# Performance work log

Measured on AMD Instinct MI355X. Metric: run time of the kernel, lower is better.

Reference implementation:

```python
import jax, jax.numpy as jnp
import numpy as np

B = 32768   # batch
D = 64      # latent_dimension_half
H = 256     # inner_dimension
T = D * (D + 1) // 2  # 2080 triangular outputs


def setup_inputs() -> dict:
    key = jax.random.key(0)
    ks = jax.random.split(key, 7)
    s = 0.05
    return {
        "x": jax.random.normal(ks[0], (B, D), dtype=jnp.float32),
        "W1": jax.random.normal(ks[1], (D, H), dtype=jnp.float32) * s,
        "b1": jax.random.normal(ks[2], (H,), dtype=jnp.float32) * s,
        "W2": jax.random.normal(ks[3], (H, H), dtype=jnp.float32) * s,
        "b2": jax.random.normal(ks[4], (H,), dtype=jnp.float32) * s,
        "W3": jax.random.normal(ks[5], (H, T), dtype=jnp.float32) * s,
        "b3": jax.random.normal(ks[6], (T,), dtype=jnp.float32) * s,
    }


def reference(x, W1, b1, W2, b2, W3, b3):
    d = x.shape[-1]  # latent_dimension_half
    h = jnp.tanh(x @ W1 + b1)
    h = jnp.tanh(h @ W2 + b2)
    t = jnp.tanh(h @ W3 + b3)  # [B, d*(d+1)/2]
    # scatter: first d entries -> diagonal (diagflat), rest -> strict upper
    # triangle in row-major order (matches torch boolean-mask assignment)
    di = np.arange(d)
    iu, ju = np.triu_indices(d, k=1)
    rows = np.concatenate([di, iu])
    cols = np.concatenate([di, ju])
    u = jnp.zeros((x.shape[0], d, d), dtype=t.dtype).at[:, rows, cols].set(t)
    # y[b] = u[b].T @ u[b]
    return jnp.einsum('bki,bkj->bij', u, u)
```

## Files before the change

kernel.cpp:

```cpp
#include <hip/hip_runtime.h>


typedef __bf16 bf16_t;
typedef bf16_t bf16x8 __attribute__((ext_vector_type(8)));
typedef float  f32x4  __attribute__((ext_vector_type(4)));

#define MFMA16(a, b, c) __builtin_amdgcn_mfma_f32_16x16x32_bf16((a), (b), (c), 0, 0, 0)

constexpr int SLOT  = 4608;
constexpr int ARENA = 73728;
constexpr int H2OFF = 147456;

__device__ __forceinline__ float fast_tanh(float x) {
  float cx = fminf(fmaxf(x, -30.0f), 30.0f);
  float t  = __expf(2.0f * cx);
  return (t - 1.0f) * __builtin_amdgcn_rcpf(t + 1.0f);
}

__device__ __forceinline__ bf16x8 zsel(bf16x8 f, bool keep) {
  union { bf16x8 v; unsigned int u[4]; } x;
  x.v = f;
  unsigned m = keep ? 0xFFFFFFFFu : 0u;
#pragma unroll
  for (int p = 0; p < 4; ++p) x.u[p] &= m;
  return x.v;
}

__device__ __forceinline__ void decode_p(int p, int& j, int& k) {
  int cc = p >> 3, e = p & 7;
  int b = 0;
  while (b < 7 && cc >= 4 * (b + 1) * (b + 2)) ++b;
  int rl  = b + 1;
  int rem = cc - 4 * b * (b + 1);
  j = 8 * b + rem / rl;
  k = (rem % rl) * 8 + e;
}

__global__ void prep_kernel(const float* __restrict__ W1, const float* __restrict__ W2,
                            const float* __restrict__ W3, const float* __restrict__ b3,
                            char* __restrict__ wsb) {
  int tid = blockIdx.x * 512 + threadIdx.x;
  bf16_t* ws = (bf16_t*)wsb;
  if (tid < 16384) {
    int n = tid >> 6, k = tid & 63;
    ws[tid] = (bf16_t)W1[k * 256 + n];
  } else if (tid < 81920) {
    int m = tid - 16384;
    int n = m >> 8, k = m & 255;
    ws[tid] = (bf16_t)W2[k * 256 + n];
  } else if (tid < 671744) {
    int m = tid - 81920;
    int t  = m >> 12;
    int r  = m & 4095;
    int kk = r >> 9;
    int g  = (r >> 7) & 3;
    int c  = (r >> 3) & 15;
    int e  = r & 7;
    int p  = t * 16 + c;
    int k  = kk * 32 + g * 8 + e;
    int j, kd;
    decode_p(p, j, kd);
    float v = 0.f;
    if (kd <= j) {
      int n_ref = (kd == j) ? j : (64 + kd * 63 - (kd * (kd - 1)) / 2 + j - kd - 1);
      v = W3[k * 2080 + n_ref];
    }
    ws[tid] = (bf16_t)v;
  } else if (tid < 674048) {
    int p = tid - 671744;
    int j, kd;
    decode_p(p, j, kd);
    float v = 0.f;
    if (kd <= j) {
      int n_ref = (kd == j) ? j : (64 + kd * 63 - (kd * (kd - 1)) / 2 + j - kd - 1);
      v = b3[n_ref];
    }
    ((float*)(wsb + 1343488))[p] = v;
  }
}

__device__ __forceinline__ void gram_store(char* slot, int sw, float* yb,
                                           int g, int c, int lane) {
  bf16x8 f0, f1, f2, f3, f2b, f3b;
#pragma unroll
  for (int ti = 0; ti < 4; ++ti) {
    int j = ti * 16 + c;
    int Q = j >> 3, s = j & 7;
    int ro = 16 * (4 * Q * (Q + 1) + s * (Q + 1));
    bf16x8 fa = *(const bf16x8*)(slot + ((ro + g * 16) ^ sw));
    if (ti == 0) f0 = zsel(fa, g * 8 <= j);
    if (ti == 1) f1 = zsel(fa, g * 8 <= j);
    if (ti == 2) f2 = fa;
    if (ti == 3) f3 = fa;
    if (ti >= 2) {
      bf16x8 fb = *(const bf16x8*)(slot + ((ro + 64 + g * 16) ^ sw));
      fb = zsel(fb, 32 + g * 8 <= j);
      if (ti == 2) f2b = fb;
      else         f3b = fb;
    }
  }

  bf16x8 fA[4] = {f0, f1, f2, f3};
  f32x4 acc[4][4];
#pragma unroll
  for (int ti = 0; ti < 4; ++ti)
#pragma unroll
    for (int tj = 0; tj < 4; ++tj) {
      f32x4 z = {0.f, 0.f, 0.f, 0.f};
      acc[ti][tj] = MFMA16(fA[ti], fA[tj], z);
    }
  acc[2][2] = MFMA16(f2b, f2b, acc[2][2]);
  acc[2][3] = MFMA16(f2b, f3b, acc[2][3]);
  acc[3][2] = MFMA16(f3b, f2b, acc[3][2]);
  acc[3][3] = MFMA16(f3b, f3b, acc[3][3]);

#pragma unroll
  for (int ti = 0; ti < 4; ++ti) {
#pragma unroll
    for (int tj = 0; tj < 4; ++tj)
#pragma unroll
      for (int r = 0; r < 4; ++r)
        *(float*)(slot + (g * 4 + r) * 256 + (tj * 16 + c) * 4) = acc[ti][tj][r];
#pragma unroll
    for (int ii = 0; ii < 4; ++ii) {
      f32x4 v = *(const f32x4*)(slot + ii * 1024 + lane * 16);
      __builtin_nontemporal_store(v, (f32x4*)(yb + ti * 1024 + ii * 256 + lane * 4));
    }
  }
}

__global__ void __launch_bounds__(768, 3)
hm_kernel(const float* __restrict__ x, const float* __restrict__ b1,
          const float* __restrict__ b2, const char* __restrict__ wsb,
          float* __restrict__ out) {
  extern __shared__ char smem[];
  const int tid  = threadIdx.x;
  const int w    = tid >> 6;
  const int lane = tid & 63;
  const int g    = lane >> 4;
  const int c    = lane & 15;
  const int blk  = blockIdx.x;

  const bf16_t* W1t = (const bf16_t*)wsb;
  const bf16_t* W2t = W1t + 16384;
  const bf16_t* W3q = W1t + 81920;
  const float*  b3p = (const float*)(wsb + 1343488);
  char* h2s = smem + H2OFF;

  float bias1[2] = {0.f, 0.f}, bias2[2] = {0.f, 0.f};
  if (w < 8) {
#pragma unroll
    for (int ni = 0; ni < 2; ++ni) {
      int n = (w * 2 + ni) * 16 + c;
      bias1[ni] = b1[n];
      bias2[ni] = b2[n];
    }
  }

#pragma unroll 1
  for (int r = 0; r < 8; ++r) {
    char* cur = smem + (r & 1) * ARENA;
    char* prv = smem + ((r & 1) ^ 1) * ARENA;
    char* xs  = cur;
    char* h1s = cur + 4096;

    if (tid < 256) {
      f32x4 v = *(const f32x4*)(x + ((size_t)blk * 128 + r * 16) * 64 + tid * 4);
      int row = tid >> 4, col = (tid & 15) * 4;
      union { bf16_t b[4]; unsigned long long u; } pk;
      pk.b[0] = (bf16_t)v[0]; pk.b[1] = (bf16_t)v[1];
      pk.b[2] = (bf16_t)v[2]; pk.b[3] = (bf16_t)v[3];
      *(unsigned long long*)(xs + ((row * 128 + col * 2) ^ ((row & 7) << 4))) = pk.u;
    }
    __syncthreads();

    if (w < 8) {
      bf16x8 a0 = *(const bf16x8*)(xs + ((c * 128 + g * 16) ^ ((c & 7) << 4)));
      bf16x8 a1 = *(const bf16x8*)(xs + ((c * 128 + 64 + g * 16) ^ ((c & 7) << 4)));
#pragma unroll
      for (int ni = 0; ni < 2; ++ni) {
        int n = (w * 2 + ni) * 16 + c;
        bf16x8 bw0 = *(const bf16x8*)(W1t + n * 64 + g * 8);
        bf16x8 bw1 = *(const bf16x8*)(W1t + n * 64 + 32 + g * 8);
        f32x4 acc = {0.f, 0.f, 0.f, 0.f};
        acc = MFMA16(a0, bw0, acc);
        acc = MFMA16(a1, bw1, acc);
#pragma unroll
        for (int rr = 0; rr < 4; ++rr) {
          int row = g * 4 + rr;
          float v = fast_tanh(acc[rr] + bias1[ni]);
          *(bf16_t*)(h1s + ((row * 512 + n * 2) ^ ((row & 7) << 4))) = (bf16_t)v;
        }
      }
    }
    __syncthreads();

    if (w < 8) {
#pragma unroll
      for (int ni = 0; ni < 2; ++ni) {
        int n = (w * 2 + ni) * 16 + c;
        f32x4 acc0 = {0.f, 0.f, 0.f, 0.f}, acc1 = {0.f, 0.f, 0.f, 0.f};
#pragma unroll
        for (int kk = 0; kk < 8; kk += 2) {
          bf16x8 a0 = *(const bf16x8*)(h1s + ((c * 512 + kk * 64 + g * 16) ^ ((c & 7) << 4)));
          bf16x8 a1 = *(const bf16x8*)(h1s + ((c * 512 + (kk + 1) * 64 + g * 16) ^ ((c & 7) << 4)));
          bf16x8 bw0 = *(const bf16x8*)(W2t + n * 256 + kk * 32 + g * 8);
          bf16x8 bw1 = *(const bf16x8*)(W2t + n * 256 + (kk + 1) * 32 + g * 8);
          acc0 = MFMA16(a0, bw0, acc0);
          acc1 = MFMA16(a1, bw1, acc1);
        }
        f32x4 acc = acc0 + acc1;
#pragma unroll
        for (int rr = 0; rr < 4; ++rr) {
          int row = g * 4 + rr;
          float v = fast_tanh(acc[rr] + bias2[ni]);
          *(bf16_t*)(h2s + ((row * 512 + n * 2) ^ ((row & 7) << 4))) = (bf16_t)v;
        }
      }
    }
    __syncthreads();

    if (w < 8) {
      bf16x8 a0 = *(const bf16x8*)(h2s + ((c * 512 + 0 * 64 + g * 16) ^ ((c & 7) << 4)));
      bf16x8 a1 = *(const bf16x8*)(h2s + ((c * 512 + 1 * 64 + g * 16) ^ ((c & 7) << 4)));
      bf16x8 a2 = *(const bf16x8*)(h2s + ((c * 512 + 2 * 64 + g * 16) ^ ((c & 7) << 4)));
      bf16x8 a3 = *(const bf16x8*)(h2s + ((c * 512 + 3 * 64 + g * 16) ^ ((c & 7) << 4)));
      bf16x8 a4 = *(const bf16x8*)(h2s + ((c * 512 + 4 * 64 + g * 16) ^ ((c & 7) << 4)));
      bf16x8 a5 = *(const bf16x8*)(h2s + ((c * 512 + 5 * 64 + g * 16) ^ ((c & 7) << 4)));
      bf16x8 a6 = *(const bf16x8*)(h2s + ((c * 512 + 6 * 64 + g * 16) ^ ((c & 7) << 4)));
      bf16x8 a7 = *(const bf16x8*)(h2s + ((c * 512 + 7 * 64 + g * 16) ^ ((c & 7) << 4)));

      char* tw = cur + (g * 4) * SLOT;
      const int swz = (g & 7) << 4;

      bf16x8 A0, A1, A2, A3, A4, A5, A6, A7; float Ab;
      bf16x8 B0, B1, B2, B3, B4, B5, B6, B7; float Bb;

#define ISSUE_T(S, TI)                                                              \
  do {                                                                              \
    int t_ = w + (TI) * 8;                                                          \
    const bf16_t* np_ = W3q + t_ * 4096 + lane * 8;                                 \
    asm volatile("global_load_dwordx4 %0, %1, off" : "=v"(S##0) : "v"(np_));            \
    asm volatile("global_load_dwordx4 %0, %1, off" : "=v"(S##1) : "v"(np_ + 512));      \
    asm volatile("global_load_dwordx4 %0, %1, off" : "=v"(S##2) : "v"(np_ + 1024));     \
    asm volatile("global_load_dwordx4 %0, %1, off" : "=v"(S##3) : "v"(np_ + 1536));     \
    asm volatile("global_load_dwordx4 %0, %1, off" : "=v"(S##4) : "v"(np_ + 2048));     \
    asm volatile("global_load_dwordx4 %0, %1, off" : "=v"(S##5) : "v"(np_ + 2560));     \
    asm volatile("global_load_dwordx4 %0, %1, off" : "=v"(S##6) : "v"(np_ + 3072));     \
    asm volatile("global_load_dwordx4 %0, %1, off" : "=v"(S##7) : "v"(np_ + 3584));     \
    asm volatile("global_load_dword %0, %1, off"   : "=v"(S##b) : "v"(b3p + t_ * 16 + c)); \
  } while (0)

#define WAIT_N(N)                                          \
  do {                                                     \
    asm volatile("s_waitcnt vmcnt(" #N ")" ::: "memory");  \
    __builtin_amdgcn_sched_barrier(0);                     \
  } while (0)

#define COMP_T(S, TI)                                                    \
  do {                                                                   \
    f32x4 acc0 = {S##b, S##b, S##b, S##b};                               \
    f32x4 acc1 = {0.f, 0.f, 0.f, 0.f};                                   \
    acc0 = MFMA16(a0, S##0, acc0); acc1 = MFMA16(a1, S##1, acc1);        \
    acc0 = MFMA16(a2, S##2, acc0); acc1 = MFMA16(a3, S##3, acc1);        \
    acc0 = MFMA16(a4, S##4, acc0); acc1 = MFMA16(a5, S##5, acc1);        \
    acc0 = MFMA16(a6, S##6, acc0); acc1 = MFMA16(a7, S##7, acc1);        \
    f32x4 accs = acc0 + acc1;                                            \
    int p_ = (w + (TI) * 8) * 16 + c;                                    \
    _Pragma("unroll")                                                    \
    for (int r_ = 0; r_ < 4; ++r_) {                                     \
      float v_ = fast_tanh(accs[r_]);                                    \
      *(bf16_t*)(tw + r_ * SLOT + ((p_ * 2) ^ swz)) = (bf16_t)v_;        \
    }                                                                    \
  } while (0)

      ISSUE_T(A, 0);
#pragma unroll 1
      for (int pr = 0; pr < 8; ++pr) {
        ISSUE_T(B, 2 * pr + 1);
        WAIT_N(9);
        COMP_T(A, 2 * pr);
        ISSUE_T(A, 2 * pr + 2);
        WAIT_N(9);
        COMP_T(B, 2 * pr + 1);
      }
      ISSUE_T(B, 17);
      WAIT_N(9);
      COMP_T(A, 16);
      WAIT_N(0);
      COMP_T(B, 17);

#undef ISSUE_T
#undef WAIT_N
#undef COMP_T
    } else if (r > 0) {
      int ww = w - 8;
#pragma unroll 1
      for (int bi = 0; bi < 4; ++bi) {
        int m = ww * 4 + bi;
        gram_store(prv + m * SLOT, ((m >> 2) & 7) << 4,
                   out + ((size_t)blk * 128 + (r - 1) * 16 + m) * 4096,
                   g, c, lane);
      }
    }
    __syncthreads();
  }

  if (w < 8) {
#pragma unroll
    for (int bi = 0; bi < 2; ++bi) {
      int m = w * 2 + bi;
      gram_store(smem + ARENA + m * SLOT, ((m >> 2) & 7) << 4,
                 out + ((size_t)blk * 128 + 7 * 16 + m) * 4096,
                 g, c, lane);
    }
  }
}

extern "C" void kernel_launch(void* const* d_in, const int* in_sizes, int n_in,
                              void* d_out, int out_size, void* d_ws, size_t ws_size,
                              hipStream_t stream) {
  (void)in_sizes; (void)n_in; (void)out_size; (void)ws_size;
  const float* x  = (const float*)d_in[0];
  const float* W1 = (const float*)d_in[1];
  const float* b1 = (const float*)d_in[2];
  const float* W2 = (const float*)d_in[3];
  const float* b2 = (const float*)d_in[4];
  const float* W3 = (const float*)d_in[5];
  const float* b3 = (const float*)d_in[6];
  char* wsb = (char*)d_ws;
  float* out = (float*)d_out;

  prep_kernel<<<1317, 512, 0, stream>>>(W1, W2, W3, b3, wsb);

  hipFuncSetAttribute((const void*)hm_kernel,
                      hipFuncAttributeMaxDynamicSharedMemorySize, 155648);
  hm_kernel<<<256, 768, 155648, stream>>>(x, b1, b2, wsb, out);
}
```

Measured before the change: 207.3 us.

## Replace block-wide barriers with LDS counter flags between producer and consumer warps

Swaps the per-stage __syncthreads between MLP warps and gram-store warps for named LDS counters: the 8 compute warps sync among themselves with atomic arrive/spin-wait, and the 4 store warps wait on per-round ready flags and signal buffer release. This lets the MLP pipeline run ahead into the next round while the store warps drain the previous arena, removing lockstep stalls. It also moves the final-round store onto the store warps. The risks are spin-wait overhead (s_sleep polling), LDS atomic traffic, and subtle memory-ordering hazards if the waitcnt/fence placement is insufficient.

```diff
diff --git a/kernel.cpp b/kernel.cpp
--- a/kernel.cpp
+++ b/kernel.cpp
@@ -10,6 +10,7 @@
 constexpr int SLOT  = 4608;
 constexpr int ARENA = 73728;
 constexpr int H2OFF = 147456;
+constexpr int CTRL  = 155648;
 
 __device__ __forceinline__ float fast_tanh(float x) {
   float cx = fminf(fmaxf(x, -30.0f), 30.0f);
@@ -34,6 +35,16 @@
   int rem = cc - 4 * b * (b + 1);
   j = 8 * b + rem / rl;
   k = (rem % rl) * 8 + e;
+}
+
+__device__ __forceinline__ void lds_arrive(unsigned* p, int lane) {
+  asm volatile("s_waitcnt lgkmcnt(0)" ::: "memory");
+  if (lane == 0) atomicAdd(p, 1u);
+}
+__device__ __forceinline__ void lds_wait(volatile unsigned* p, unsigned tgt) {
+  while (*p < tgt) __builtin_amdgcn_s_sleep(2);
+  asm volatile("" ::: "memory");
+  __builtin_amdgcn_sched_barrier(0);
 }
 
 __global__ void prep_kernel(const float* __restrict__ W1, const float* __restrict__ W2,
@@ -146,56 +157,59 @@
   const bf16_t* W3q = W1t + 81920;
   const float*  b3p = (const float*)(wsb + 1343488);
   char* h2s = smem + H2OFF;
-
-  float bias1[2] = {0.f, 0.f}, bias2[2] = {0.f, 0.f};
+  unsigned* ctrl = (unsigned*)(smem + CTRL);
+
+  if (tid < 40) ctrl[tid] = 0;
+  __syncthreads();
+
   if (w < 8) {
+    float bias1[2], bias2[2];
 #pragma unroll
     for (int ni = 0; ni < 2; ++ni) {
       int n = (w * 2 + ni) * 16 + c;
       bias1[ni] = b1[n];
       bias2[ni] = b2[n];
     }
-  }
 
 #pragma unroll 1
-  for (int r = 0; r < 8; ++r) {
-    char* cur = smem + (r & 1) * ARENA;
-    char* prv = smem + ((r & 1) ^ 1) * ARENA;
-    char* xs  = cur;
-    char* h1s = cur + 4096;
-
-    if (tid < 256) {
-      f32x4 v = *(const f32x4*)(x + ((size_t)blk * 128 + r * 16) * 64 + tid * 4);
-      int row = tid >> 4, col = (tid & 15) * 4;
-      union { bf16_t b[4]; unsigned long long u; } pk;
-      pk.b[0] = (bf16_t)v[0]; pk.b[1] = (bf16_t)v[1];
-      pk.b[2] = (bf16_t)v[2]; pk.b[3] = (bf16_t)v[3];
-      *(unsigned long long*)(xs + ((row * 128 + col * 2) ^ ((row & 7) << 4))) = pk.u;
-    }
-    __syncthreads();
-
-    if (w < 8) {
-      bf16x8 a0 = *(const bf16x8*)(xs + ((c * 128 + g * 16) ^ ((c & 7) << 4)));
-      bf16x8 a1 = *(const bf16x8*)(xs + ((c * 128 + 64 + g * 16) ^ ((c & 7) << 4)));
-#pragma unroll
-      for (int ni = 0; ni < 2; ++ni) {
-        int n = (w * 2 + ni) * 16 + c;
-        bf16x8 bw0 = *(const bf16x8*)(W1t + n * 64 + g * 8);
-        bf16x8 bw1 = *(const bf16x8*)(W1t + n * 64 + 32 + g * 8);
-        f32x4 acc = {0.f, 0.f, 0.f, 0.f};
-        acc = MFMA16(a0, bw0, acc);
-        acc = MFMA16(a1, bw1, acc);
-#pragma unroll
-        for (int rr = 0; rr < 4; ++rr) {
-          int row = g * 4 + rr;
-          float v = fast_tanh(acc[rr] + bias1[ni]);
-          *(bf16_t*)(h1s + ((row * 512 + n * 2) ^ ((row & 7) << 4))) = (bf16_t)v;
+    for (int r = 0; r < 8; ++r) {
+      char* cur = smem + (r & 1) * ARENA;
+      char* xs  = cur;
+      char* h1s = cur + 4096;
+
+      if (r >= 2) lds_wait(&ctrl[32 + (r - 2)], 4);
+
+      if (tid < 256) {
+        f32x4 v = *(const f32x4*)(x + ((size_t)blk * 128 + r * 16) * 64 + tid * 4);
+        int row = tid >> 4, col = (tid & 15) * 4;
+        union { bf16_t b[4]; unsigned long long u; } pk;
+        pk.b[0] = (bf16_t)v[0]; pk.b[1] = (bf16_t)v[1];
+        pk.b[2] = (bf16_t)v[2]; pk.b[3] = (bf16_t)v[3];
+        *(unsigned long long*)(xs + ((row * 128 + col * 2) ^ ((row & 7) << 4))) = pk.u;
+      }
+      lds_arrive(&ctrl[r * 3 + 0], lane); lds_wait(&ctrl[r * 3 + 0], 8);
+
+      {
+        bf16x8 a0 = *(const bf16x8*)(xs + ((c * 128 + g * 16) ^ ((c & 7) << 4)));
+        bf16x8 a1 = *(const bf16x8*)(xs + ((c * 128 + 64 + g * 16) ^ ((c & 7) << 4)));
+#pragma unroll
+        for (int ni = 0; ni < 2; ++ni) {
+          int n = (w * 2 + ni) * 16 + c;
+          bf16x8 bw0 = *(const bf16x8*)(W1t + n * 64 + g * 8);
+          bf16x8 bw1 = *(const bf16x8*)(W1t + n * 64 + 32 + g * 8);
+          f32x4 acc = {0.f, 0.f, 0.f, 0.f};
+          acc = MFMA16(a0, bw0, acc);
+          acc = MFMA16(a1, bw1, acc);
+#pragma unroll
+          for (int rr = 0; rr < 4; ++rr) {
+            int row = g * 4 + rr;
+            float v = fast_tanh(acc[rr] + bias1[ni]);
+            *(bf16_t*)(h1s + ((row * 512 + n * 2) ^ ((row & 7) << 4))) = (bf16_t)v;
+          }
         }
       }
-    }
-    __syncthreads();
-
-    if (w < 8) {
+      lds_arrive(&ctrl[r * 3 + 1], lane); lds_wait(&ctrl[r * 3 + 1], 8);
+
 #pragma unroll
       for (int ni = 0; ni < 2; ++ni) {
         int n = (w * 2 + ni) * 16 + c;
@@ -217,24 +231,23 @@
           *(bf16_t*)(h2s + ((row * 512 + n * 2) ^ ((row & 7) << 4))) = (bf16_t)v;
         }
       }
-    }
-    __syncthreads();
-
-    if (w < 8) {
-      bf16x8 a0 = *(const bf16x8*)(h2s + ((c * 512 + 0 * 64 + g * 16) ^ ((c & 7) << 4)));
-      bf16x8 a1 = *(const bf16x8*)(h2s + ((c * 512 + 1 * 64 + g * 16) ^ ((c & 7) << 4)));
-      bf16x8 a2 = *(const bf16x8*)(h2s + ((c * 512 + 2 * 64 + g * 16) ^ ((c & 7) << 4)));
-      bf16x8 a3 = *(const bf16x8*)(h2s + ((c * 512 + 3 * 64 + g * 16) ^ ((c & 7) << 4)));
-      bf16x8 a4 = *(const bf16x8*)(h2s + ((c * 512 + 4 * 64 + g * 16) ^ ((c & 7) << 4)));
-      bf16x8 a5 = *(const bf16x8*)(h2s + ((c * 512 + 5 * 64 + g * 16) ^ ((c & 7) << 4)));
-      bf16x8 a6 = *(const bf16x8*)(h2s + ((c * 512 + 6 * 64 + g * 16) ^ ((c & 7) << 4)));
-      bf16x8 a7 = *(const bf16x8*)(h2s + ((c * 512 + 7 * 64 + g * 16) ^ ((c & 7) << 4)));
-
-      char* tw = cur + (g * 4) * SLOT;
-      const int swz = (g & 7) << 4;
-
-      bf16x8 A0, A1, A2, A3, A4, A5, A6, A7; float Ab;
-      bf16x8 B0, B1, B2, B3, B4, B5, B6, B7; float Bb;
+      lds_arrive(&ctrl[r * 3 + 2], lane); lds_wait(&ctrl[r * 3 + 2], 8);
+
+      {
+        bf16x8 a0 = *(const bf16x8*)(h2s + ((c * 512 + 0 * 64 + g * 16) ^ ((c & 7) << 4)));
+        bf16x8 a1 = *(const bf16x8*)(h2s + ((c * 512 + 1 * 64 + g * 16) ^ ((c & 7) << 4)));
+        bf16x8 a2 = *(const bf16x8*)(h2s + ((c * 512 + 2 * 64 + g * 16) ^ ((c & 7) << 4)));
+        bf16x8 a3 = *(const bf16x8*)(h2s + ((c * 512 + 3 * 64 + g * 16) ^ ((c & 7) << 4)));
+        bf16x8 a4 = *(const bf16x8*)(h2s + ((c * 512 + 4 * 64 + g * 16) ^ ((c & 7) << 4)));
+        bf16x8 a5 = *(const bf16x8*)(h2s + ((c * 512 + 5 * 64 + g * 16) ^ ((c & 7) << 4)));
+        bf16x8 a6 = *(const bf16x8*)(h2s + ((c * 512 + 6 * 64 + g * 16) ^ ((c & 7) << 4)));
+        bf16x8 a7 = *(const bf16x8*)(h2s + ((c * 512 + 7 * 64 + g * 16) ^ ((c & 7) << 4)));
+
+        char* tw = cur + (g * 4) * SLOT;
+        const int swz = (g & 7) << 4;
+
+        bf16x8 A0, A1, A2, A3, A4, A5, A6, A7; float Ab;
+        bf16x8 B0, B1, B2, B3, B4, B5, B6, B7; float Bb;
 
 #define ISSUE_T(S, TI)                                                              \
   do {                                                                              \
@@ -274,45 +287,42 @@
     }                                                                    \
   } while (0)
 
-      ISSUE_T(A, 0);
+        ISSUE_T(A, 0);
 #pragma unroll 1
-      for (int pr = 0; pr < 8; ++pr) {
-        ISSUE_T(B, 2 * pr + 1);
+        for (int pr = 0; pr < 8; ++pr) {
+          ISSUE_T(B, 2 * pr + 1);
+          WAIT_N(9);
+          COMP_T(A, 2 * pr);
+          ISSUE_T(A, 2 * pr + 2);
+          WAIT_N(9);
+          COMP_T(B, 2 * pr + 1);
+        }
+        ISSUE_T(B, 17);
         WAIT_N(9);
-        COMP_T(A, 2 * pr);
-        ISSUE_T(A, 2 * pr + 2);
-        WAIT_N(9);
-        COMP_T(B, 2 * pr + 1);
-      }
-      ISSUE_T(B, 17);
-      WAIT_N(9);
-      COMP_T(A, 16);
-      WAIT_N(0);
-      COMP_T(B, 17);
+        COMP_T(A, 16);
+        WAIT_N(0);
+        COMP_T(B, 17);
 
 #undef ISSUE_T
 #undef WAIT_N
 #undef COMP_T
-    } else if (r > 0) {
-      int ww = w - 8;
+      }
+      lds_arrive(&ctrl[24 + r], lane);
+    }
+  } else {
+    int ww = w - 8;
+#pragma unroll 1
+    for (int r = 0; r < 8; ++r) {
+      lds_wait(&ctrl[24 + r], 8);
+      char* arena = smem + (r & 1) * ARENA;
 #pragma unroll 1
       for (int bi = 0; bi < 4; ++bi) {
         int m = ww * 4 + bi;
-        gram_store(prv + m * SLOT, ((m >> 2) & 7) << 4,
-                   out + ((size_t)blk * 128 + (r - 1) * 16 + m) * 4096,
+        gram_store(arena + m * SLOT, ((m >> 2) & 7) << 4,
+                   out + ((size_t)blk * 128 + r * 16 + m) * 4096,
                    g, c, lane);
       }
-    }
-    __syncthreads();
-  }
-
-  if (w < 8) {
-#pragma unroll
-    for (int bi = 0; bi < 2; ++bi) {
-      int m = w * 2 + bi;
-      gram_store(smem + ARENA + m * SLOT, ((m >> 2) & 7) << 4,
-                 out + ((size_t)blk * 128 + 7 * 16 + m) * 4096,
-                 g, c, lane);
+      lds_arrive(&ctrl[32 + r], lane);
     }
   }
 }
@@ -334,6 +344,6 @@
   prep_kernel<<<1317, 512, 0, stream>>>(W1, W2, W3, b3, wsb);
 
   hipFuncSetAttribute((const void*)hm_kernel,
-                      hipFuncAttributeMaxDynamicSharedMemorySize, 155648);
-  hm_kernel<<<256, 768, 155648, stream>>>(x, b1, b2, wsb, out);
-}
+                      hipFuncAttributeMaxDynamicSharedMemorySize, 155904);
+  hm_kernel<<<256, 768, 155904, stream>>>(x, b1, b2, wsb, out);
+}
```

Result: faster. 191.1 us (-7.8%).
